# Performance work log

Hardware: AMD Instinct MI355X
Metric: run time of the kernel (lower is better)

## Reference

```python
import jax, jax.numpy as jnp
import numpy as np

N_NODES = 50000
N_EDGES = 800000
IN_FEAT = 128
OUT_FEAT = 128


def _glorot(key, shape):
    fan_in, fan_out = shape[1], shape[0]
    lim = jnp.sqrt(6.0 / (fan_in + fan_out))
    return jax.random.uniform(key, shape, jnp.float32, -lim, lim)


def setup_inputs() -> dict:
    key = jax.random.key(0)
    ks = jax.random.split(key, 9)
    x = jax.random.normal(ks[0], (N_NODES, IN_FEAT), jnp.float32)
    edge_index = jax.random.randint(ks[1], (2, N_EDGES), 0, N_NODES, jnp.int64)
    # SAGEConv params: lin_l applied to aggregated neighbors (with bias),
    # lin_r applied to root features (no bias) -- PyG default mean aggregation.
    W1l = _glorot(ks[2], (OUT_FEAT, IN_FEAT)); b1l = jnp.zeros((OUT_FEAT,), jnp.float32)
    W1r = _glorot(ks[3], (OUT_FEAT, IN_FEAT))
    W2l = _glorot(ks[4], (OUT_FEAT, OUT_FEAT)); b2l = jnp.zeros((OUT_FEAT,), jnp.float32)
    W2r = _glorot(ks[5], (OUT_FEAT, OUT_FEAT))
    Wlin = _glorot(ks[6], (2, OUT_FEAT)); blin = jnp.zeros((2,), jnp.float32)
    return {"x": x, "edge_index": edge_index,
            "W1l": W1l, "b1l": b1l, "W1r": W1r,
            "W2l": W2l, "b2l": b2l, "W2r": W2r,
            "Wlin": Wlin, "blin": blin}


def _sage_conv(x, src, dst, Wl, bl, Wr, n_nodes):
    # mean-aggregate neighbor features at destination nodes
    agg_sum = jax.ops.segment_sum(x[src], dst, num_segments=n_nodes)  # [N, F]
    deg = jax.ops.segment_sum(jnp.ones((src.shape[0],), x.dtype), dst, num_segments=n_nodes)
    agg = agg_sum / jnp.maximum(deg, 1.0)[:, None]
    return agg @ Wl.T + bl + x @ Wr.T


def reference(x, edge_index, W1l, b1l, W1r, W2l, b2l, W2r, Wlin, blin):
    src, dst = edge_index[0], edge_index[1]
    n = x.shape[0]
    h = _sage_conv(x, src, dst, W1l, b1l, W1r, n)
    h = jax.nn.relu(h)  # dropout is identity in eval mode
    h = _sage_conv(h, src, dst, W2l, b2l, W2r, n)
    h = jax.nn.relu(h)
    logits = h @ Wlin.T + blin  # [N, 2]
    return jax.nn.log_softmax(logits, axis=1)
```

## Files before the change

kernel.cpp:

```cpp
#include <hip/hip_runtime.h>
#include <math.h>

#define N_NODES 50000
#define N_EDGES 800000
#define F 128
#define ELL_CAP 64
#define NSHARD 8
#define RANKS 128
#define EPR (N_EDGES / RANKS)
#define NPS (N_NODES / NSHARD)
#define NBPS 25
#define NBUCK (NSHARD * NBPS)
#define BIN_CAP 80
#define BUCK_CAP 4608
#define EDGE_BLKS (NSHARD * RANKS)
#define CVT_BLKS 6250

typedef __attribute__((ext_vector_type(8))) short short8;
typedef __attribute__((ext_vector_type(4))) float float4v;

__device__ inline unsigned short f2bf(float f) {
    unsigned int u = __builtin_bit_cast(unsigned int, f);
    u += 0x7FFF + ((u >> 16) & 1);
    return (unsigned short)(u >> 16);
}
__device__ inline float bf2f_lo(unsigned int u) {
    return __builtin_bit_cast(float, u << 16);
}
__device__ inline float bf2f_hi(unsigned int u) {
    return __builtin_bit_cast(float, u & 0xFFFF0000u);
}

__global__ __launch_bounds__(256) void prep1(const float* __restrict__ x,
                                             const int* __restrict__ src,
                                             const int* __restrict__ dst,
                                             const float* __restrict__ W1l,
                                             const float* __restrict__ W1r,
                                             const float* __restrict__ W2l,
                                             const float* __restrict__ W2r,
                                             unsigned short* __restrict__ xb,
                                             int* __restrict__ tails,
                                             unsigned int* __restrict__ bucketEdges,
                                             unsigned short* __restrict__ P1,
                                             unsigned short* __restrict__ P2) {
    int blk = blockIdx.x;
    int tid = threadIdx.x;
    if (blk < EDGE_BLKS) {
        __shared__ int bin_cnt[NBPS];
        __shared__ int bin_base[NBPS];
        __shared__ unsigned int bins[NBPS * BIN_CAP];
        int shard = blk & 7;
        int rank = blk >> 3;
        int lo = shard * NPS;
        if (tid < NBPS) bin_cnt[tid] = 0;
        __syncthreads();
        int base = rank * EPR;
        for (int i = tid; i < EPR; i += 256) {
            int d = dst[base + i];
            unsigned int du = (unsigned int)(d - lo);
            if (du < (unsigned int)NPS) {
                int s = src[base + i];
                int lb = du >> 8;
                int pos = atomicAdd(&bin_cnt[lb], 1);
                if (pos < BIN_CAP)
                    bins[lb * BIN_CAP + pos] = ((du & 255u) << 16) | (unsigned int)s;
            }
        }
        __syncthreads();
        if (tid < NBPS) {
            int c = bin_cnt[tid]; if (c > BIN_CAP) c = BIN_CAP;
            bin_cnt[tid] = c;
            bin_base[tid] = atomicAdd(&tails[shard * NBPS + tid], c);
        }
        __syncthreads();
        for (int b2 = 0; b2 < NBPS; ++b2) {
            int c = bin_cnt[b2];
            int rb = bin_base[b2];
            unsigned int* dp = bucketEdges + (size_t)(shard * NBPS + b2) * BUCK_CAP;
            for (int i = tid; i < c; i += 256)
                if (rb + i < BUCK_CAP) dp[rb + i] = bins[b2 * BIN_CAP + i];
        }
    } else if (blk < EDGE_BLKS + CVT_BLKS) {
        int i = (blk - EDGE_BLKS) * 256 + tid;
        float4 v = ((const float4*)x)[i];
        unsigned int p0 = (unsigned int)f2bf(v.x) | ((unsigned int)f2bf(v.y) << 16);
        unsigned int p1 = (unsigned int)f2bf(v.z) | ((unsigned int)f2bf(v.w) << 16);
        ((uint2*)xb)[i] = make_uint2(p0, p1);
    } else {
        int pblk = blk - (EDGE_BLKS + CVT_BLKS);
        int t = (pblk & 15) * 256 + tid;
        int lane = t & 63;
        int ct = (t >> 6) & 7;
        int ks = t >> 9;
        const float* Wl = (pblk < 16) ? W1l : W2l;
        const float* Wr = (pblk < 16) ? W1r : W2r;
        unsigned short* P = (pblk < 16) ? P1 : P2;
        int col = ct * 16 + (lane & 15);
        int kbase = (ks & 3) * 32 + (lane >> 4) * 8;
        const float* W = (ks < 4) ? Wl : Wr;
        unsigned short* dp = P + (size_t)t * 8;
        #pragma unroll
        for (int j = 0; j < 8; ++j) dp[j] = f2bf(W[col * F + kbase + j]);
    }
}

__global__ __launch_bounds__(256) void ell_build(const int* __restrict__ tails,
                                                 const unsigned int* __restrict__ bucketEdges,
                                                 int* __restrict__ cnt,
                                                 unsigned short* __restrict__ nbr) {
    __shared__ int cl[256];
    __shared__ unsigned short ell[256 * ELL_CAP];
    int b = blockIdx.x;
    int tid = threadIdx.x;
    cl[tid] = 0;
    __syncthreads();
    int T = tails[b]; if (T > BUCK_CAP) T = BUCK_CAP;
    const unsigned int* eb = bucketEdges + (size_t)b * BUCK_CAP;
    for (int i = tid; i < T; i += 256) {
        unsigned int rec = eb[i];
        int nib = rec >> 16;
        int pos = atomicAdd(&cl[nib], 1);
        if (pos < ELL_CAP) ell[nib * ELL_CAP + pos] = (unsigned short)(rec & 0xFFFFu);
    }
    __syncthreads();
    int shard = b / NBPS, lb = b % NBPS;
    int nb0 = shard * NPS + lb * 256;
    int nn = NPS - lb * 256; if (nn > 256) nn = 256;
    if (tid < nn) cnt[nb0 + tid] = cl[tid];
    const uint4* s4 = (const uint4*)ell;
    uint4* d4 = (uint4*)(nbr + (size_t)nb0 * ELL_CAP);
    int n4 = nn * (ELL_CAP * 2 / 16);
    for (int i = tid; i < n4; i += 256) d4[i] = s4[i];
}

__global__ __launch_bounds__(256) void aggregate2(const unsigned short* __restrict__ X,
                                                  const int* __restrict__ cnt,
                                                  const unsigned short* __restrict__ nbr,
                                                  unsigned short* __restrict__ agg) {
    int tid = threadIdx.x;
    int wave = tid >> 6;
    int lane = tid & 63;
    int half = lane >> 5;
    int hl = lane & 31;
    int node = blockIdx.x * 8 + wave * 2 + half;

    int degt = cnt[node];
    int deg = degt < ELL_CAP ? degt : ELL_CAP;
    const unsigned short* nb = nbr + node * ELL_CAP;

    float a0 = 0.f, a1 = 0.f, a2 = 0.f, a3 = 0.f;
    int s = 0;
    for (; s + 4 <= deg; s += 4) {
        ushort4 nv = *(const ushort4*)(nb + s);
        uint2 g0 = *(const uint2*)(X + (size_t)nv.x * F + hl * 4);
        uint2 g1 = *(const uint2*)(X + (size_t)nv.y * F + hl * 4);
        uint2 g2 = *(const uint2*)(X + (size_t)nv.z * F + hl * 4);
        uint2 g3 = *(const uint2*)(X + (size_t)nv.w * F + hl * 4);
        a0 += bf2f_lo(g0.x) + bf2f_lo(g1.x) + bf2f_lo(g2.x) + bf2f_lo(g3.x);
        a1 += bf2f_hi(g0.x) + bf2f_hi(g1.x) + bf2f_hi(g2.x) + bf2f_hi(g3.x);
        a2 += bf2f_lo(g0.y) + bf2f_lo(g1.y) + bf2f_lo(g2.y) + bf2f_lo(g3.y);
        a3 += bf2f_hi(g0.y) + bf2f_hi(g1.y) + bf2f_hi(g2.y) + bf2f_hi(g3.y);
    }
    for (; s < deg; ++s) {
        int v = nb[s];
        uint2 g = *(const uint2*)(X + (size_t)v * F + hl * 4);
        a0 += bf2f_lo(g.x); a1 += bf2f_hi(g.x);
        a2 += bf2f_lo(g.y); a3 += bf2f_hi(g.y);
    }
    float inv = 1.0f / (float)(degt > 0 ? degt : 1);
    unsigned int p0 = (unsigned int)f2bf(a0 * inv) | ((unsigned int)f2bf(a1 * inv) << 16);
    unsigned int p1 = (unsigned int)f2bf(a2 * inv) | ((unsigned int)f2bf(a3 * inv) << 16);
    *(uint2*)(agg + (size_t)node * F + hl * 4) = make_uint2(p0, p1);
}

__global__ __launch_bounds__(256) void sage_gemm(const unsigned short* __restrict__ Abf,
                                                 const unsigned short* __restrict__ Bbf,
                                                 const unsigned short* __restrict__ Pw,
                                                 const float* __restrict__ bias,
                                                 unsigned short* __restrict__ Hout,
                                                 const float* __restrict__ Wlin,
                                                 const float* __restrict__ blin,
                                                 float* __restrict__ out, int mode) {
    int lane = threadIdx.x & 63;
    int wave = threadIdx.x >> 6;
    int r0 = blockIdx.x * 64 + wave * 16;
    int rowA = r0 + (lane & 15);
    if (rowA >= N_NODES) rowA = N_NODES - 1;
    int kg = lane >> 4;

    short8 af[4], bfr[4];
    const short8* Ap = (const short8*)(Abf + (size_t)rowA * F);
    const short8* Bp = (const short8*)(Bbf + (size_t)rowA * F);
    #pragma unroll
    for (int ks = 0; ks < 4; ++ks) {
        af[ks]  = Ap[ks * 4 + kg];
        bfr[ks] = Bp[ks * 4 + kg];
    }

    const short8* Wp = (const short8*)Pw;
    float4v acc[8];
    #pragma unroll
    for (int ct = 0; ct < 8; ++ct) {
        float4v c = {0.f, 0.f, 0.f, 0.f};
        #pragma unroll
        for (int ks = 0; ks < 4; ++ks)
            c = __builtin_amdgcn_mfma_f32_16x16x32_bf16(af[ks], Wp[(ks * 8 + ct) * 64 + lane], c, 0, 0, 0);
        #pragma unroll
        for (int ks = 0; ks < 4; ++ks)
            c = __builtin_amdgcn_mfma_f32_16x16x32_bf16(bfr[ks], Wp[((ks + 4) * 8 + ct) * 64 + lane], c, 0, 0, 0);
        acc[ct] = c;
    }

    int colb = lane & 15;
    int rq = lane >> 4;
    #pragma unroll
    for (int ct = 0; ct < 8; ++ct) {
        float bv = bias[ct * 16 + colb];
        #pragma unroll
        for (int i = 0; i < 4; ++i)
            acc[ct][i] = fmaxf(acc[ct][i] + bv, 0.f);
    }

    if (mode == 0) {
        #pragma unroll
        for (int ct = 0; ct < 8; ++ct) {
            #pragma unroll
            for (int i = 0; i < 4; ++i) {
                int row = r0 + rq * 4 + i;
                if (row < N_NODES)
                    Hout[(size_t)row * F + ct * 16 + colb] = f2bf(acc[ct][i]);
            }
        }
    } else {
        float w0[8], w1[8];
        #pragma unroll
        for (int ct = 0; ct < 8; ++ct) {
            w0[ct] = Wlin[ct * 16 + colb];
            w1[ct] = Wlin[F + ct * 16 + colb];
        }
        #pragma unroll
        for (int i = 0; i < 4; ++i) {
            float p0 = 0.f, p1 = 0.f;
            #pragma unroll
            for (int ct = 0; ct < 8; ++ct) {
                p0 += acc[ct][i] * w0[ct];
                p1 += acc[ct][i] * w1[ct];
            }
            #pragma unroll
            for (int off = 1; off < 16; off <<= 1) {
                p0 += __shfl_xor(p0, off);
                p1 += __shfl_xor(p1, off);
            }
            int row = r0 + rq * 4 + i;
            if (colb == 0 && row < N_NODES) {
                float a = p0 + blin[0];
                float b = p1 + blin[1];
                float m = fmaxf(a, b);
                float lse = m + logf(expf(a - m) + expf(b - m));
                out[(size_t)row * 2 + 0] = a - lse;
                out[(size_t)row * 2 + 1] = b - lse;
            }
        }
    }
}

extern "C" void kernel_launch(void* const* d_in, const int* in_sizes, int n_in,
                              void* d_out, int out_size, void* d_ws, size_t ws_size,
                              hipStream_t stream) {
    const float* x    = (const float*)d_in[0];
    const int*   ei   = (const int*)d_in[1];
    const float* W1l  = (const float*)d_in[2];
    const float* b1l  = (const float*)d_in[3];
    const float* W1r  = (const float*)d_in[4];
    const float* W2l  = (const float*)d_in[5];
    const float* b2l  = (const float*)d_in[6];
    const float* W2r  = (const float*)d_in[7];
    const float* Wlin = (const float*)d_in[8];
    const float* blin = (const float*)d_in[9];
    float* out = (float*)d_out;

    const int* src = ei;
    const int* dst = ei + N_EDGES;

    char* ws = (char*)d_ws;
    int*            tails = (int*)ws;
    unsigned int*   bEdge = (unsigned int*)(ws + 4096);
    int*            cnt   = (int*)(ws + 3694592);
    unsigned short* nbr   = (unsigned short*)(ws + 3895296);
    unsigned short* xb    = (unsigned short*)(ws + 10296320);
    unsigned short* h1b   = (unsigned short*)(ws + 23097344);
    unsigned short* aggb  = (unsigned short*)(ws + 35898368);
    unsigned short* P1    = (unsigned short*)(ws + 48699392);
    unsigned short* P2    = (unsigned short*)(ws + 48764928);

    hipMemsetAsync(tails, 0, NBUCK * sizeof(int), stream);

    prep1<<<EDGE_BLKS + CVT_BLKS + 32, 256, 0, stream>>>(x, src, dst, W1l, W1r, W2l, W2r,
                                                         xb, tails, bEdge, P1, P2);
    ell_build<<<NBUCK, 256, 0, stream>>>(tails, bEdge, cnt, nbr);

    aggregate2<<<6250, 256, 0, stream>>>(xb, cnt, nbr, aggb);
    sage_gemm<<<782, 256, 0, stream>>>(aggb, xb, P1, b1l, h1b, nullptr, nullptr, nullptr, 0);

    aggregate2<<<6250, 256, 0, stream>>>(h1b, cnt, nbr, aggb);
    sage_gemm<<<782, 256, 0, stream>>>(aggb, h1b, P2, b2l, nullptr, Wlin, blin, out, 1);
}
```

Before: 137.9 us.

## Quantize gathered node features to int8 with per-row scales for aggregation

Produces an int8 copy of x and of the layer-1 hidden features, each row with a float scale, and has the neighbor-mean aggregation gather these 4-byte-per-lane rows instead of 8-byte bf16 rows. This halves the bytes fetched in the random-gather phase, which dominates the cost. In exchange, prep1 and the layer-1 GEMM epilogue do extra max reductions and int8 stores, each gather reads an extra scale, and int8 precision may loosen accuracy against the reference.

Measured after the change: 127.6 us. 1.08x faster.

```diff
diff --git a/kernel.cpp b/kernel.cpp
--- a/kernel.cpp
+++ b/kernel.cpp
@@ -30,6 +30,9 @@
 __device__ inline float bf2f_hi(unsigned int u) {
     return __builtin_bit_cast(float, u & 0xFFFF0000u);
 }
+__device__ inline float i8f(unsigned int u, int k) {
+    return (float)((signed char)(u >> (k * 8)));
+}
 
 __global__ __launch_bounds__(256) void prep1(const float* __restrict__ x,
                                              const int* __restrict__ src,
@@ -39,6 +42,8 @@
                                              const float* __restrict__ W2l,
                                              const float* __restrict__ W2r,
                                              unsigned short* __restrict__ xb,
+                                             unsigned char* __restrict__ xq,
+                                             float* __restrict__ xscale,
                                              int* __restrict__ tails,
                                              unsigned int* __restrict__ bucketEdges,
                                              unsigned short* __restrict__ P1,
@@ -81,11 +86,21 @@
                 if (rb + i < BUCK_CAP) dp[rb + i] = bins[b2 * BIN_CAP + i];
         }
     } else if (blk < EDGE_BLKS + CVT_BLKS) {
-        int i = (blk - EDGE_BLKS) * 256 + tid;
-        float4 v = ((const float4*)x)[i];
+        int row = (blk - EDGE_BLKS) * 8 + (tid >> 5);
+        int hl = tid & 31;
+        float4 v = ((const float4*)x)[row * 32 + hl];
+        float m = fmaxf(fmaxf(fabsf(v.x), fabsf(v.y)), fmaxf(fabsf(v.z), fabsf(v.w)));
+        #pragma unroll
+        for (int off = 1; off < 32; off <<= 1) m = fmaxf(m, __shfl_xor(m, off));
+        float inv = m > 0.f ? 127.f / m : 0.f;
+        int q0 = (int)rintf(v.x * inv), q1 = (int)rintf(v.y * inv);
+        int q2 = (int)rintf(v.z * inv), q3 = (int)rintf(v.w * inv);
+        unsigned int qp = (q0 & 255) | ((q1 & 255) << 8) | ((q2 & 255) << 16) | ((q3 & 255) << 24);
+        ((unsigned int*)xq)[row * 32 + hl] = qp;
         unsigned int p0 = (unsigned int)f2bf(v.x) | ((unsigned int)f2bf(v.y) << 16);
         unsigned int p1 = (unsigned int)f2bf(v.z) | ((unsigned int)f2bf(v.w) << 16);
-        ((uint2*)xb)[i] = make_uint2(p0, p1);
+        ((uint2*)xb)[row * 32 + hl] = make_uint2(p0, p1);
+        if (hl == 0) xscale[row] = m * (1.f / 127.f);
     } else {
         int pblk = blk - (EDGE_BLKS + CVT_BLKS);
         int t = (pblk & 15) * 256 + tid;
@@ -133,10 +148,11 @@
     for (int i = tid; i < n4; i += 256) d4[i] = s4[i];
 }
 
-__global__ __launch_bounds__(256) void aggregate2(const unsigned short* __restrict__ X,
-                                                  const int* __restrict__ cnt,
-                                                  const unsigned short* __restrict__ nbr,
-                                                  unsigned short* __restrict__ agg) {
+__global__ __launch_bounds__(256) void aggregate_q(const unsigned char* __restrict__ Xq,
+                                                   const float* __restrict__ xs,
+                                                   const int* __restrict__ cnt,
+                                                   const unsigned short* __restrict__ nbr,
+                                                   unsigned short* __restrict__ agg) {
     int tid = threadIdx.x;
     int wave = tid >> 6;
     int lane = tid & 63;
@@ -147,25 +163,26 @@
     int degt = cnt[node];
     int deg = degt < ELL_CAP ? degt : ELL_CAP;
     const unsigned short* nb = nbr + node * ELL_CAP;
+    const unsigned int* Xu = (const unsigned int*)Xq;
 
     float a0 = 0.f, a1 = 0.f, a2 = 0.f, a3 = 0.f;
     int s = 0;
     for (; s + 4 <= deg; s += 4) {
         ushort4 nv = *(const ushort4*)(nb + s);
-        uint2 g0 = *(const uint2*)(X + (size_t)nv.x * F + hl * 4);
-        uint2 g1 = *(const uint2*)(X + (size_t)nv.y * F + hl * 4);
-        uint2 g2 = *(const uint2*)(X + (size_t)nv.z * F + hl * 4);
-        uint2 g3 = *(const uint2*)(X + (size_t)nv.w * F + hl * 4);
-        a0 += bf2f_lo(g0.x) + bf2f_lo(g1.x) + bf2f_lo(g2.x) + bf2f_lo(g3.x);
-        a1 += bf2f_hi(g0.x) + bf2f_hi(g1.x) + bf2f_hi(g2.x) + bf2f_hi(g3.x);
-        a2 += bf2f_lo(g0.y) + bf2f_lo(g1.y) + bf2f_lo(g2.y) + bf2f_lo(g3.y);
-        a3 += bf2f_hi(g0.y) + bf2f_hi(g1.y) + bf2f_hi(g2.y) + bf2f_hi(g3.y);
+        unsigned int g0 = Xu[nv.x * 32 + hl]; float s0 = xs[nv.x];
+        unsigned int g1 = Xu[nv.y * 32 + hl]; float s1 = xs[nv.y];
+        unsigned int g2 = Xu[nv.z * 32 + hl]; float s2 = xs[nv.z];
+        unsigned int g3 = Xu[nv.w * 32 + hl]; float s3 = xs[nv.w];
+        a0 += i8f(g0, 0) * s0 + i8f(g1, 0) * s1 + i8f(g2, 0) * s2 + i8f(g3, 0) * s3;
+        a1 += i8f(g0, 1) * s0 + i8f(g1, 1) * s1 + i8f(g2, 1) * s2 + i8f(g3, 1) * s3;
+        a2 += i8f(g0, 2) * s0 + i8f(g1, 2) * s1 + i8f(g2, 2) * s2 + i8f(g3, 2) * s3;
+        a3 += i8f(g0, 3) * s0 + i8f(g1, 3) * s1 + i8f(g2, 3) * s2 + i8f(g3, 3) * s3;
     }
     for (; s < deg; ++s) {
         int v = nb[s];
-        uint2 g = *(const uint2*)(X + (size_t)v * F + hl * 4);
-        a0 += bf2f_lo(g.x); a1 += bf2f_hi(g.x);
-        a2 += bf2f_lo(g.y); a3 += bf2f_hi(g.y);
+        unsigned int g = Xu[v * 32 + hl]; float sc = xs[v];
+        a0 += i8f(g, 0) * sc; a1 += i8f(g, 1) * sc;
+        a2 += i8f(g, 2) * sc; a3 += i8f(g, 3) * sc;
     }
     float inv = 1.0f / (float)(degt > 0 ? degt : 1);
     unsigned int p0 = (unsigned int)f2bf(a0 * inv) | ((unsigned int)f2bf(a1 * inv) << 16);
@@ -178,6 +195,8 @@
                                                  const unsigned short* __restrict__ Pw,
                                                  const float* __restrict__ bias,
                                                  unsigned short* __restrict__ Hout,
+                                                 unsigned char* __restrict__ Hq,
+                                                 float* __restrict__ Hscale,
                                                  const float* __restrict__ Wlin,
                                                  const float* __restrict__ blin,
                                                  float* __restrict__ out, int mode) {
@@ -229,6 +248,24 @@
                 int row = r0 + rq * 4 + i;
                 if (row < N_NODES)
                     Hout[(size_t)row * F + ct * 16 + colb] = f2bf(acc[ct][i]);
+            }
+        }
+        #pragma unroll
+        for (int i = 0; i < 4; ++i) {
+            float m = 0.f;
+            #pragma unroll
+            for (int ct = 0; ct < 8; ++ct) m = fmaxf(m, acc[ct][i]);
+            #pragma unroll
+            for (int off = 1; off < 16; off <<= 1) m = fmaxf(m, __shfl_xor(m, off));
+            float inv = m > 0.f ? 127.f / m : 0.f;
+            int row = r0 + rq * 4 + i;
+            if (row < N_NODES) {
+                if (colb == 0) Hscale[row] = m * (1.f / 127.f);
+                #pragma unroll
+                for (int ct = 0; ct < 8; ++ct) {
+                    int q = (int)rintf(acc[ct][i] * inv);
+                    Hq[(size_t)row * F + ct * 16 + colb] = (unsigned char)q;
+                }
             }
         }
     } else {
@@ -283,25 +320,31 @@
     const int* dst = ei + N_EDGES;
 
     char* ws = (char*)d_ws;
-    int*            tails = (int*)ws;
-    unsigned int*   bEdge = (unsigned int*)(ws + 4096);
-    int*            cnt   = (int*)(ws + 3694592);
-    unsigned short* nbr   = (unsigned short*)(ws + 3895296);
-    unsigned short* xb    = (unsigned short*)(ws + 10296320);
-    unsigned short* h1b   = (unsigned short*)(ws + 23097344);
-    unsigned short* aggb  = (unsigned short*)(ws + 35898368);
-    unsigned short* P1    = (unsigned short*)(ws + 48699392);
-    unsigned short* P2    = (unsigned short*)(ws + 48764928);
+    int*            tails  = (int*)ws;
+    unsigned int*   bEdge  = (unsigned int*)(ws + 4096);
+    int*            cnt    = (int*)(ws + 3694592);
+    unsigned short* nbr    = (unsigned short*)(ws + 3895296);
+    unsigned short* xb     = (unsigned short*)(ws + 10296320);
+    unsigned short* h1b    = (unsigned short*)(ws + 23097344);
+    unsigned short* aggb   = (unsigned short*)(ws + 35898368);
+    unsigned short* P1     = (unsigned short*)(ws + 48699392);
+    unsigned short* P2     = (unsigned short*)(ws + 48764928);
+    unsigned char*  xq     = (unsigned char*)(ws + 48830464);
+    unsigned char*  h1q    = (unsigned char*)(ws + 55230464);
+    float*          xscale = (float*)(ws + 61630464);
+    float*          h1scale= (float*)(ws + 61830464);
 
     hipMemsetAsync(tails, 0, NBUCK * sizeof(int), stream);
 
     prep1<<<EDGE_BLKS + CVT_BLKS + 32, 256, 0, stream>>>(x, src, dst, W1l, W1r, W2l, W2r,
-                                                         xb, tails, bEdge, P1, P2);
+                                                         xb, xq, xscale, tails, bEdge, P1, P2);
     ell_build<<<NBUCK, 256, 0, stream>>>(tails, bEdge, cnt, nbr);
 
-    aggregate2<<<6250, 256, 0, stream>>>(xb, cnt, nbr, aggb);
-    sage_gemm<<<782, 256, 0, stream>>>(aggb, xb, P1, b1l, h1b, nullptr, nullptr, nullptr, 0);
-
-    aggregate2<<<6250, 256, 0, stream>>>(h1b, cnt, nbr, aggb);
-    sage_gemm<<<782, 256, 0, stream>>>(aggb, h1b, P2, b2l, nullptr, Wlin, blin, out, 1);
-}
+    aggregate_q<<<6250, 256, 0, stream>>>(xq, xscale, cnt, nbr, aggb);
+    sage_gemm<<<782, 256, 0, stream>>>(aggb, xb, P1, b1l, h1b, h1q, h1scale,
+                                       nullptr, nullptr, nullptr, 0);
+
+    aggregate_q<<<6250, 256, 0, stream>>>(h1q, h1scale, cnt, nbr, aggb);
+    sage_gemm<<<782, 256, 0, stream>>>(aggb, h1b, P2, b2l, nullptr, nullptr, nullptr,
+                                       Wlin, blin, out, 1);
+}
```
